# Kernel tuning notes

Hardware: AMD Instinct MI355X
Metric: run time of the kernel (lower is better)

Reference implementation:

```python
import jax, jax.numpy as jnp
import numpy as np

CORE_DIM = 128
MEMORY_SLOTS = 64
B, S = 4, 4096


def setup_inputs() -> dict:
    key = jax.random.key(0)
    k1, k2, k3, k4, k5 = jax.random.split(key, 5)
    x = jax.random.normal(k1, (B, S, CORE_DIM), dtype=jnp.float32)
    memory_keys = jax.random.normal(k2, (MEMORY_SLOTS, CORE_DIM), dtype=jnp.float32)
    memory_ops = jax.random.normal(k3, (MEMORY_SLOTS, CORE_DIM, CORE_DIM), dtype=jnp.float32)
    # nn.Linear(core_dim, core_dim): weight [out, in], bias [out]
    bound = 1.0 / np.sqrt(CORE_DIM)
    Wq = jax.random.uniform(k4, (CORE_DIM, CORE_DIM), minval=-bound, maxval=bound, dtype=jnp.float32)
    bq = jax.random.uniform(k5, (CORE_DIM,), minval=-bound, maxval=bound, dtype=jnp.float32)
    return {"input_tensor": x, "memory_keys": memory_keys, "memory_ops": memory_ops, "Wq": Wq, "bq": bq}


def reference(input_tensor, memory_keys, memory_ops, Wq, bq):
    dim = input_tensor.shape[-1]
    # query projection: x @ Wq^T + bq
    queries = jnp.einsum('bsd,ed->bse', input_tensor, Wq) + bq
    # soft attention over memory slots
    attn_logits = jnp.einsum('bsd,md->bsm', queries, memory_keys)
    attn_weights = jax.nn.softmax(attn_logits / jnp.sqrt(jnp.float32(dim)), axis=-1)
    # fused: (sum_m attn[bsm] * ops[m]) @ x[bs]  == sum_m attn[bsm] * (ops[m] @ x[bs])
    processed = jnp.einsum('bsm,mde,bse->bsd', attn_weights, memory_ops, input_tensor)
    return processed
```

## Files before the change

kernel.cpp:

```cpp
#include <hip/hip_runtime.h>

typedef __bf16 bf16x8 __attribute__((ext_vector_type(8)));
typedef float f32x4 __attribute__((ext_vector_type(4)));
typedef unsigned int uint4v __attribute__((ext_vector_type(4)));
typedef unsigned short ushort_t;
typedef unsigned int uint_t;

#define RS 0.08838834764831845f

__device__ __forceinline__ ushort_t f2bf(float f) {
    uint_t u = __float_as_uint(f);
    u += 0x7FFFu + ((u >> 16) & 1u);
    return (ushort_t)(u >> 16);
}
__device__ __forceinline__ uint_t pack2(float a, float b) {
    return (uint_t)f2bf(a) | ((uint_t)f2bf(b) << 16);
}
union U4B8 { uint4v u; bf16x8 b; };
__device__ __forceinline__ bf16x8 as_bf(uint4v u) { U4B8 x; x.u = u; return x.b; }

__device__ __forceinline__ int xfrag(int f, int lane) {
    return f * 1072 + ((lane >> 4) * 272) + ((lane & 15) * 16);
}

__global__ __launch_bounds__(256) void prep_kernel(
    const float* __restrict__ ops, const float* __restrict__ keys,
    const float* __restrict__ Wq, const float* __restrict__ bq,
    uint4v* __restrict__ ops_sw, ushort_t* __restrict__ kp_sw,
    float* __restrict__ cb)
{
    const int tid = threadIdx.x;
    const int b = blockIdx.x;
    if (b >= 64) {
        int g = (b - 64) * 256 + tid;
        int L = g & 63, dt = (g >> 6) & 7, ks = (g >> 9) & 3, m = g >> 11;
        int d = dt * 16 + (L & 15);
        int e0 = ks * 32 + ((L >> 4) << 3);
        const float4* s = (const float4*)(ops + (((size_t)(m * 128 + d)) << 7) + e0);
        float4 v0 = s[0], v1 = s[1];
        uint4v o = { pack2(v0.x, v0.y), pack2(v0.z, v0.w),
                     pack2(v1.x, v1.y), pack2(v1.z, v1.w) };
        ops_sw[g] = o;
    } else {
        __shared__ float red[256];
        const int m = b;
        const int d = tid & 127, eh = tid >> 7;
        const float* kr = keys + m * 128 + eh * 64;
        const float* wc = Wq + (size_t)(eh * 64) * 128 + d;
        float acc = 0.f;
        #pragma unroll 8
        for (int e = 0; e < 64; ++e)
            acc = fmaf(kr[e], wc[(size_t)e * 128], acc);
        red[tid] = acc;
        __syncthreads();
        if (tid < 128) {
            float v = red[tid] + red[tid + 128];
            int ki = d >> 5, qq = (d >> 3) & 3, j = d & 7;
            kp_sw[((((ki * 4 + (m >> 4)) * 64) + (qq * 16 + (m & 15))) << 3) | j] = f2bf(v);
        } else if (tid >= 192) {
            int lane = tid - 192;
            float p = keys[m * 128 + lane] * bq[lane]
                    + keys[m * 128 + 64 + lane] * bq[64 + lane];
            #pragma unroll
            for (int off = 1; off < 64; off <<= 1) p += __shfl_xor(p, off);
            if (lane == 0) cb[m] = p;
        }
    }
}

__global__ __launch_bounds__(256, 2) void main_kernel(
    const float* __restrict__ x, const float* __restrict__ cb,
    const ushort_t* __restrict__ kp_sw, const uint4v* __restrict__ ops_sw,
    float* __restrict__ out)
{
    __shared__ __align__(16) unsigned char xs[17152];
    __shared__ float attn_f[64 * 68];

    const int tid = threadIdx.x;
    const int lane = tid & 63;
    const int w = tid >> 6;
    const int q = lane >> 4;
    const int l15 = lane & 15;
    const int tb = blockIdx.x >> 1;
    const int dh = blockIdx.x & 1;
    const int t0 = tb * 64;
    const int dtw = dh * 4 + w;

    {
        const float4* x4 = (const float4*)(x + (size_t)t0 * 128);
        #pragma unroll
        for (int it = 0; it < 4; ++it) {
            int i = it * 256 + tid;
            int t = i >> 4, kc = i & 15;
            float4 a = x4[t * 32 + kc * 2];
            float4 b2 = x4[t * 32 + kc * 2 + 1];
            uint4v o = { pack2(a.x, a.y), pack2(a.z, a.w),
                         pack2(b2.x, b2.y), pack2(b2.z, b2.w) };
            *(uint4v*)(xs + ((t >> 4) * 4 + (kc >> 2)) * 1072
                          + (kc & 3) * 272 + (t & 15) * 16) = o;
        }
    }
    __syncthreads();

    {
        f32x4 L0 = {0,0,0,0}, L1 = {0,0,0,0}, L2 = {0,0,0,0}, L3 = {0,0,0,0};
        const uint4v* kpf = (const uint4v*)kp_sw;
        #pragma unroll
        for (int ki = 0; ki < 4; ++ki) {
            bf16x8 a = *(const bf16x8*)(xs + xfrag(w * 4 + ki, lane));
            L0 = __builtin_amdgcn_mfma_f32_16x16x32_bf16(a, as_bf(kpf[(ki*4+0)*64 + lane]), L0, 0,0,0);
            L1 = __builtin_amdgcn_mfma_f32_16x16x32_bf16(a, as_bf(kpf[(ki*4+1)*64 + lane]), L1, 0,0,0);
            L2 = __builtin_amdgcn_mfma_f32_16x16x32_bf16(a, as_bf(kpf[(ki*4+2)*64 + lane]), L2, 0,0,0);
            L3 = __builtin_amdgcn_mfma_f32_16x16x32_bf16(a, as_bf(kpf[(ki*4+3)*64 + lane]), L3, 0,0,0);
        }
        float c0 = cb[l15], c1 = cb[16 + l15], c2 = cb[32 + l15], c3 = cb[48 + l15];
        #pragma unroll
        for (int r = 0; r < 4; ++r) {
            float v0 = (L0[r] + c0) * RS;
            float v1 = (L1[r] + c1) * RS;
            float v2 = (L2[r] + c2) * RS;
            float v3 = (L3[r] + c3) * RS;
            float mx = fmaxf(fmaxf(v0, v1), fmaxf(v2, v3));
            #pragma unroll
            for (int off = 1; off < 16; off <<= 1) mx = fmaxf(mx, __shfl_xor(mx, off));
            float e0 = __expf(v0 - mx), e1 = __expf(v1 - mx),
                  e2 = __expf(v2 - mx), e3 = __expf(v3 - mx);
            float sm = e0 + e1 + e2 + e3;
            #pragma unroll
            for (int off = 1; off < 16; off <<= 1) sm += __shfl_xor(sm, off);
            float inv = 1.0f / sm;
            int t = w * 16 + q * 4 + r;
            attn_f[(     l15) * 68 + t] = e0 * inv;
            attn_f[(16 + l15) * 68 + t] = e1 * inv;
            attn_f[(32 + l15) * 68 + t] = e2 * inv;
            attn_f[(48 + l15) * 68 + t] = e3 * inv;
        }
    }

    bf16x8 A[4][4];
    #pragma unroll
    for (int tf = 0; tf < 4; ++tf)
        #pragma unroll
        for (int ki = 0; ki < 4; ++ki)
            A[tf][ki] = *(const bf16x8*)(xs + xfrag(tf * 4 + ki, lane));

    __syncthreads();

    const uint4v* ob = ops_sw + (size_t)dtw * 64 + lane;
    f32x4 C[4] = {};
    uint4v B[4][4];
    #pragma unroll
    for (int ki = 0; ki < 4; ++ki) {
        B[0][ki] = ob[ki * 512];
        B[1][ki] = ob[2048 + ki * 512];
    }

    #pragma unroll 4
    for (int ml = 0; ml < 64; ++ml) {
        const int cur = ml & 3, nxt = (ml + 2) & 3;
        if (ml < 62) {
            const uint4v* pn = ob + (size_t)(ml + 2) * 2048;
            #pragma unroll
            for (int ki = 0; ki < 4; ++ki) B[nxt][ki] = pn[ki * 512];
        }
        f32x4 S[4] = {};
        #pragma unroll
        for (int ki = 0; ki < 4; ++ki) {
            bf16x8 bfrag = as_bf(B[cur][ki]);
            #pragma unroll
            for (int tf = 0; tf < 4; ++tf)
                S[tf] = __builtin_amdgcn_mfma_f32_16x16x32_bf16(A[tf][ki], bfrag, S[tf], 0,0,0);
        }
        #pragma unroll
        for (int tf = 0; tf < 4; ++tf) {
            f32x4 af = *(const f32x4*)&attn_f[ml * 68 + tf * 16 + q * 4];
            #pragma unroll
            for (int r = 0; r < 4; ++r)
                C[tf][r] = fmaf(af[r], S[tf][r], C[tf][r]);
        }
    }

    float* op = out + (size_t)t0 * 128 + dh * 64 + w * 16 + l15;
    #pragma unroll
    for (int tf = 0; tf < 4; ++tf)
        #pragma unroll
        for (int r = 0; r < 4; ++r)
            op[(size_t)(tf * 16 + q * 4 + r) * 128] = C[tf][r];
}

extern "C" void kernel_launch(void* const* d_in, const int* in_sizes, int n_in,
                              void* d_out, int out_size, void* d_ws, size_t ws_size,
                              hipStream_t stream)
{
    const float* x    = (const float*)d_in[0];
    const float* keys = (const float*)d_in[1];
    const float* ops  = (const float*)d_in[2];
    const float* Wq   = (const float*)d_in[3];
    const float* bq   = (const float*)d_in[4];
    float* out = (float*)d_out;

    char* ws = (char*)d_ws;
    uint4v*   ops_sw = (uint4v*)ws;
    ushort_t* kp_sw  = (ushort_t*)(ws + 2097152);
    float*    cb     = (float*)(ws + 2097152 + 16384);

    prep_kernel<<<576, 256, 0, stream>>>(ops, keys, Wq, bq, ops_sw, kp_sw, cb);
    main_kernel<<<512, 256, 0, stream>>>(x, cb, kp_sw, ops_sw, out);
}
```

Before: 108.5 us.

## Split memory slots across block pair with atomic accumulation instead of splitting output dims

The two blocks that share a 64-token tile now each take half of the 64 memory slots and all 128 output dims, where before each took half the output dims and all slots. Each wave computes two 16-wide dim tiles per slot, and the attention buffer shrinks to 32 slots. Partial results are combined with float atomicAdd into an output zeroed by an added memset. This halves the serial slot loop and doubles MFMA work per iteration for more ILP. In exchange it adds atomic traffic, a memset launch, and summation order that is no longer deterministic.

```diff
diff --git a/kernel.cpp b/kernel.cpp
--- a/kernel.cpp
+++ b/kernel.cpp
@@ -74,7 +74,7 @@
     float* __restrict__ out)
 {
     __shared__ __align__(16) unsigned char xs[17152];
-    __shared__ float attn_f[64 * 68];
+    __shared__ float attn_f[32 * 68];
 
     const int tid = threadIdx.x;
     const int lane = tid & 63;
@@ -82,9 +82,8 @@
     const int q = lane >> 4;
     const int l15 = lane & 15;
     const int tb = blockIdx.x >> 1;
-    const int dh = blockIdx.x & 1;
+    const int kb = blockIdx.x & 1;
     const int t0 = tb * 64;
-    const int dtw = dh * 4 + w;
 
     {
         const float4* x4 = (const float4*)(x + (size_t)t0 * 128);
@@ -130,10 +129,10 @@
             for (int off = 1; off < 16; off <<= 1) sm += __shfl_xor(sm, off);
             float inv = 1.0f / sm;
             int t = w * 16 + q * 4 + r;
-            attn_f[(     l15) * 68 + t] = e0 * inv;
-            attn_f[(16 + l15) * 68 + t] = e1 * inv;
-            attn_f[(32 + l15) * 68 + t] = e2 * inv;
-            attn_f[(48 + l15) * 68 + t] = e3 * inv;
+            float ea = (kb == 0) ? e0 : e2;
+            float eb = (kb == 0) ? e1 : e3;
+            attn_f[(     l15) * 68 + t] = ea * inv;
+            attn_f[(16 + l15) * 68 + t] = eb * inv;
         }
     }
 
@@ -146,46 +145,55 @@
 
     __syncthreads();
 
-    const uint4v* ob = ops_sw + (size_t)dtw * 64 + lane;
-    f32x4 C[4] = {};
-    uint4v B[4][4];
+    const uint4v* ob0 = ops_sw + (size_t)(kb * 32) * 2048 + (size_t)(w * 2    ) * 64 + lane;
+    const uint4v* ob1 = ops_sw + (size_t)(kb * 32) * 2048 + (size_t)(w * 2 + 1) * 64 + lane;
+    f32x4 C[4][2] = {};
+    uint4v B[2][2][4];
     #pragma unroll
     for (int ki = 0; ki < 4; ++ki) {
-        B[0][ki] = ob[ki * 512];
-        B[1][ki] = ob[2048 + ki * 512];
-    }
-
-    #pragma unroll 4
-    for (int ml = 0; ml < 64; ++ml) {
-        const int cur = ml & 3, nxt = (ml + 2) & 3;
-        if (ml < 62) {
-            const uint4v* pn = ob + (size_t)(ml + 2) * 2048;
-            #pragma unroll
-            for (int ki = 0; ki < 4; ++ki) B[nxt][ki] = pn[ki * 512];
-        }
-        f32x4 S[4] = {};
+        B[0][0][ki] = ob0[ki * 512];
+        B[0][1][ki] = ob1[ki * 512];
+    }
+
+    #pragma unroll 2
+    for (int ml = 0; ml < 32; ++ml) {
+        const int cur = ml & 1, nxt = cur ^ 1;
+        const size_t off = (size_t)((ml < 31) ? ml + 1 : 31) * 2048;
         #pragma unroll
         for (int ki = 0; ki < 4; ++ki) {
-            bf16x8 bfrag = as_bf(B[cur][ki]);
-            #pragma unroll
-            for (int tf = 0; tf < 4; ++tf)
-                S[tf] = __builtin_amdgcn_mfma_f32_16x16x32_bf16(A[tf][ki], bfrag, S[tf], 0,0,0);
+            B[nxt][0][ki] = ob0[off + ki * 512];
+            B[nxt][1][ki] = ob1[off + ki * 512];
+        }
+        f32x4 S[4][2] = {};
+        #pragma unroll
+        for (int ki = 0; ki < 4; ++ki) {
+            bf16x8 b0 = as_bf(B[cur][0][ki]);
+            bf16x8 b1 = as_bf(B[cur][1][ki]);
+            #pragma unroll
+            for (int tf = 0; tf < 4; ++tf) {
+                S[tf][0] = __builtin_amdgcn_mfma_f32_16x16x32_bf16(A[tf][ki], b0, S[tf][0], 0,0,0);
+                S[tf][1] = __builtin_amdgcn_mfma_f32_16x16x32_bf16(A[tf][ki], b1, S[tf][1], 0,0,0);
+            }
         }
         #pragma unroll
         for (int tf = 0; tf < 4; ++tf) {
             f32x4 af = *(const f32x4*)&attn_f[ml * 68 + tf * 16 + q * 4];
             #pragma unroll
-            for (int r = 0; r < 4; ++r)
-                C[tf][r] = fmaf(af[r], S[tf][r], C[tf][r]);
-        }
-    }
-
-    float* op = out + (size_t)t0 * 128 + dh * 64 + w * 16 + l15;
+            for (int dd = 0; dd < 2; ++dd)
+                #pragma unroll
+                for (int r = 0; r < 4; ++r)
+                    C[tf][dd][r] = fmaf(af[r], S[tf][dd][r], C[tf][dd][r]);
+        }
+    }
+
+    float* op = out + (size_t)t0 * 128 + w * 32 + l15;
     #pragma unroll
     for (int tf = 0; tf < 4; ++tf)
         #pragma unroll
-        for (int r = 0; r < 4; ++r)
-            op[(size_t)(tf * 16 + q * 4 + r) * 128] = C[tf][r];
+        for (int dd = 0; dd < 2; ++dd)
+            #pragma unroll
+            for (int r = 0; r < 4; ++r)
+                atomicAdd(&op[(size_t)(tf * 16 + q * 4 + r) * 128 + dd * 16], C[tf][dd][r]);
 }
 
 extern "C" void kernel_launch(void* const* d_in, const int* in_sizes, int n_in,
@@ -204,6 +212,7 @@
     ushort_t* kp_sw  = (ushort_t*)(ws + 2097152);
     float*    cb     = (float*)(ws + 2097152 + 16384);
 
+    hipMemsetAsync(d_out, 0, (size_t)out_size * sizeof(float), stream);
     prep_kernel<<<576, 256, 0, stream>>>(ops, keys, Wq, bq, ops_sw, kp_sw, cb);
     main_kernel<<<512, 256, 0, stream>>>(x, cb, kp_sw, ops_sw, out);
 }
```

Result: slower. 118.9 us (+9.6%).
